# Kernel optimization log

Measured on AMD Instinct MI355X. Metric: run time of the kernel, lower is better.

The kernel has to match this reference:

```python
import jax, jax.numpy as jnp
import numpy as np

PATCH = 4  # patch_size from init_kwargs


def setup_inputs() -> dict:
    key = jax.random.key(0)
    x = jax.random.normal(key, (16, 64, 256, 256), dtype=jnp.float32)
    return {"x": x}


def reference(x):
    # Original torch loop: k-th patch has row-block index advancing fastest
    # (i += p each step, j += p on wrap), so patch order is (j_block outer,
    # i_block inner). Each patch is x[:, :, i:i+p, j:j+p].flatten(1), i.e.
    # channel-major, then patch-row, then patch-col.
    N, C, H, W = x.shape
    p = PATCH
    Hp, Wp = H // p, W // p
    # [N,C,Hp,p,Wp,p] -> [N,Wp,Hp,C,p,p] -> [N, Wp*Hp, C*p*p]
    out = (x.reshape(N, C, Hp, p, Wp, p)
            .transpose(0, 4, 2, 1, 3, 5)
            .reshape(N, Wp * Hp, C * p * p))
    ori_shape = jnp.asarray((N, C, H, W), dtype=jnp.int32)
    return out, ori_shape
```

## Files before the change

### kernel.cpp

```cpp
#include <hip/hip_runtime.h>


constexpr int N  = 16;
constexpr int C  = 64;
constexpr int H  = 256;
constexpr int W  = 256;
constexpr int P  = 4;
constexpr int HP = H / P;
constexpr int WP = W / P;
constexpr int W4 = W / 4;

__global__ __launch_bounds__(256) void patch_embed_kernel(
    const float* __restrict__ x, float* __restrict__ out)
{
    const int t = blockIdx.x * 256 + threadIdx.x;
    const int wp = t & 63;
    const int hp = (t >> 6) & 63;
    const int c  = (t >> 12) & 63;
    const int n  = t >> 18;

    const float4* __restrict__ x4 = (const float4*)x;
    float4* __restrict__ o4       = (float4*)out;

    const long bin = ((long)((n * C + c) * H + hp * P)) * W4 + wp;
    const long bout = ((long)(n * (WP * HP) + wp * HP + hp)) * (C * P * P / 4) + c * 4;

    float4 r0 = x4[bin + 0 * W4];
    float4 r1 = x4[bin + 1 * W4];
    float4 r2 = x4[bin + 2 * W4];
    float4 r3 = x4[bin + 3 * W4];
    o4[bout + 0] = r0;
    o4[bout + 1] = r1;
    o4[bout + 2] = r2;
    o4[bout + 3] = r3;
}

__global__ void tail_kernel(float* __restrict__ out, int off)
{
    if (threadIdx.x == 0) {
        out[off + 0] = (float)N;
        out[off + 1] = (float)C;
        out[off + 2] = (float)H;
        out[off + 3] = (float)W;
    }
}

extern "C" void kernel_launch(void* const* d_in, const int* in_sizes, int n_in,
                              void* d_out, int out_size, void* d_ws, size_t ws_size,
                              hipStream_t stream)
{
    const float* x = (const float*)d_in[0];
    float* out     = (float*)d_out;

    const int total  = N * C * HP * WP;
    const int blocks = total / 256;

    patch_embed_kernel<<<blocks, 256, 0, stream>>>(x, out);
    tail_kernel<<<1, 64, 0, stream>>>(out, out_size - 4);
}
```

Before: 476.8 us.

## Stage patch tiles through LDS to make output writes fully contiguous

Each block now loads a tile of 16 patches across all channels into shared memory, then writes whole 4KB tokens contiguously. Previously each thread wrote 64B fragments to addresses far apart, which gave scattered partial-line stores. The LDS index is XOR-swizzled to avoid bank conflicts. This costs 64KB of LDS per block and a barrier, which limits how many blocks can be resident on a CU.

```diff
diff --git a/kernel.cpp b/kernel.cpp
--- a/kernel.cpp
+++ b/kernel.cpp
@@ -9,30 +9,42 @@
 constexpr int HP = H / P;
 constexpr int WP = W / P;
 constexpr int W4 = W / 4;
+constexpr int WT = 16;
+constexpr int TOK4 = C * P * P / 4;
 
-__global__ __launch_bounds__(256) void patch_embed_kernel(
-    const float* __restrict__ x, float* __restrict__ out)
+__global__ __launch_bounds__(512) void patch_embed_kernel(
+    const float4* __restrict__ x4, float4* __restrict__ o4)
 {
-    const int t = blockIdx.x * 256 + threadIdx.x;
-    const int wp = t & 63;
-    const int hp = (t >> 6) & 63;
-    const int c  = (t >> 12) & 63;
-    const int n  = t >> 18;
+    __shared__ float4 lds[WT * TOK4];
 
-    const float4* __restrict__ x4 = (const float4*)x;
-    float4* __restrict__ o4       = (float4*)out;
+    const int t   = threadIdx.x;
+    const int bid = blockIdx.x;
+    const int wt  = bid & 3;
+    const int hp  = (bid >> 2) & 63;
+    const int n   = bid >> 8;
+    const int wp0 = wt * WT;
 
-    const long bin = ((long)((n * C + c) * H + hp * P)) * W4 + wp;
-    const long bout = ((long)(n * (WP * HP) + wp * HP + hp)) * (C * P * P / 4) + c * 4;
+#pragma unroll
+    for (int i = 0; i < 8; ++i) {
+        const int f    = i * 512 + t;
+        const int c4pi = f >> 4;
+        const int v    = f & 15;
+        const int c    = c4pi >> 2;
+        const int pi   = c4pi & 3;
+        const int in_idx = ((n * C + c) * H + hp * P + pi) * W4 + wp0 + v;
+        lds[v * TOK4 + (c4pi ^ v)] = x4[in_idx];
+    }
 
-    float4 r0 = x4[bin + 0 * W4];
-    float4 r1 = x4[bin + 1 * W4];
-    float4 r2 = x4[bin + 2 * W4];
-    float4 r3 = x4[bin + 3 * W4];
-    o4[bout + 0] = r0;
-    o4[bout + 1] = r1;
-    o4[bout + 2] = r2;
-    o4[bout + 3] = r3;
+    __syncthreads();
+
+#pragma unroll
+    for (int i = 0; i < 8; ++i) {
+        const int g = i * 512 + t;
+        const int v = g >> 8;
+        const int j = g & 255;
+        const int out_idx = (n * (WP * HP) + (wp0 + v) * HP + hp) * TOK4 + j;
+        o4[out_idx] = lds[v * TOK4 + (j ^ v)];
+    }
 }
 
 __global__ void tail_kernel(float* __restrict__ out, int off)
@@ -49,12 +61,11 @@
                               void* d_out, int out_size, void* d_ws, size_t ws_size,
                               hipStream_t stream)
 {
-    const float* x = (const float*)d_in[0];
-    float* out     = (float*)d_out;
+    const float4* x4 = (const float4*)d_in[0];
+    float4* o4       = (float4*)d_out;
+    float* out       = (float*)d_out;
 
-    const int total  = N * C * HP * WP;
-    const int blocks = total / 256;
-
-    patch_embed_kernel<<<blocks, 256, 0, stream>>>(x, out);
+    const int blocks = N * HP * (WP / WT);
+    patch_embed_kernel<<<blocks, 512, 0, stream>>>(x4, o4);
     tail_kernel<<<1, 64, 0, stream>>>(out, out_size - 4);
 }
```

After: 432.9 us. 1.1x faster.
